# Optimization experiments

Measured on AMD Instinct MI355X. Metric: run time of the kernel, lower is better.

Reference implementation:

```python
import jax, jax.numpy as jnp
import numpy as np

F_DIM = 32          # phi_feature_dim
P = 128             # preselection_ap (spatial H=W)
NU = 4              # num_users
N1 = NU - 1         # n_cat1 == n_cat2
N3 = (NU - 1) ** 2  # n_cat3


def setup_inputs() -> dict:
    key = jax.random.key(0)
    k1, k2, k3, k4, k5 = jax.random.split(key, 5)
    B, CIN = 32, 8
    phi_input = jax.random.normal(k1, (B, CIN, P, P), dtype=jnp.float32)
    W1 = jax.random.normal(k2, (4 * F_DIM, CIN), dtype=jnp.float32) * 0.1
    b1 = jax.random.normal(k3, (4 * F_DIM,), dtype=jnp.float32) * 0.1
    W3 = jax.random.normal(k4, (4 * F_DIM, 4 * F_DIM), dtype=jnp.float32) * 0.1
    b3 = jax.random.normal(k5, (4 * F_DIM,), dtype=jnp.float32) * 0.1
    ex = jnp.ones((P, P), dtype=jnp.float32) - jnp.eye(P, dtype=jnp.float32)
    return {"phi_input": phi_input, "W1": W1, "b1": b1, "W3": W3, "b3": b3, "ex": ex}


def _conv1x1(x, W, b):
    # 1x1 conv == channel matmul: [b,c,h,w] x [o,c] -> [b,o,h,w]
    return jnp.einsum('bchw,oc->bohw', x, W) + b[None, :, None, None]


def _postprocess(r, ex):
    f = F_DIM
    c0 = r[:, :f]
    c1 = jnp.einsum('ph,bchw->bcpw', ex, r[:, f:2 * f]) / N1
    c2 = jnp.einsum('bchw,wq->bchq', r[:, 2 * f:3 * f], ex) / N1
    c3 = jnp.einsum('ph,bchw,wq->bcpq', ex, r[:, 3 * f:4 * f], ex) / N3
    return jnp.concatenate((c0, c1, c2, c3), axis=1)


def reference(phi_input, W1, b1, W3, b3, ex):
    r = jax.nn.relu(_conv1x1(phi_input, W1, b1))
    r = _postprocess(r, ex)
    r = jax.nn.relu(_conv1x1(r, W3, b3))
    r = _postprocess(r, ex)
    return r
```

## Files before the change

kernel.cpp:

```cpp
#include <hip/hip_runtime.h>
#include <stdint.h>

#define BATCH 32
#define CIN   8
#define NCH   128
#define PP    128
#define NSTRIP 8
#define KSTRIP 16

typedef __attribute__((ext_vector_type(8))) short    bf16x8;
typedef __attribute__((ext_vector_type(4))) float    f32x4;

__device__ __forceinline__ float bf2f(unsigned short u) {
    union { unsigned int i; float f; } x; x.i = ((unsigned int)u) << 16; return x.f;
}
__device__ __forceinline__ unsigned short f2bf(float f) {
    union { float f; unsigned int i; } x; x.f = f;
    unsigned int r = x.i + 0x7fffu + ((x.i >> 16) & 1u);
    return (unsigned short)(r >> 16);
}
__device__ __forceinline__ unsigned int pk2(float a, float b) {
    return (unsigned int)f2bf(a) | ((unsigned int)f2bf(b) << 16);
}

#define SWZB(row, cb) (((row) << 8) + ((cb) ^ (((row) & 7) << 4)))

__global__ __launch_bounds__(512, 4) void k1_sums(const float* __restrict__ phi,
        const float* __restrict__ W1, const float* __restrict__ b1,
        float* __restrict__ RS1t, float* __restrict__ CS1p) {
    __shared__ float cs_f[128 * 132];
    __shared__ unsigned short phi_b[2][1024];
    int bx = blockIdx.x;
    int b = bx >> 3, strip = bx & 7;
    int p0 = strip * 16;
    int tid = threadIdx.x;
    int wv = tid >> 6, l = tid & 63, lr = l & 15, lg = l >> 4;
    int c0 = wv * 16 + lg * 4;

    bf16x8 w1fr = {0, 0, 0, 0, 0, 0, 0, 0};
    if (lg == 0) {
        int cc = wv * 16 + lr;
        float4 wa = *(const float4*)(W1 + cc * 8);
        float4 wb = *(const float4*)(W1 + cc * 8 + 4);
        w1fr[0] = (short)f2bf(wa.x); w1fr[1] = (short)f2bf(wa.y);
        w1fr[2] = (short)f2bf(wa.z); w1fr[3] = (short)f2bf(wa.w);
        w1fr[4] = (short)f2bf(wb.x); w1fr[5] = (short)f2bf(wb.y);
        w1fr[6] = (short)f2bf(wb.z); w1fr[7] = (short)f2bf(wb.w);
    }
    f32x4 binit = {b1[c0], b1[c0 + 1], b1[c0 + 2], b1[c0 + 3]};
    if (tid < 128) {
        bf16x8 pv;
        #pragma unroll
        for (int ci = 0; ci < 8; ++ci)
            pv[ci] = (short)f2bf(phi[((size_t)(b * CIN + ci) * PP + p0) * PP + tid]);
        *(bf16x8*)(phi_b[0] + tid * 8) = pv;
    }
    __syncthreads();

    f32x4 cs_acc[8];
    #pragma unroll
    for (int i = 0; i < 8; ++i) { f32x4 z = {0.f, 0.f, 0.f, 0.f}; cs_acc[i] = z; }

    int cur = 0;
    for (int r = 0; r < 16; ++r) {
        int p = p0 + r;
        float pfv[8];
        if (r < 15 && tid < 128) {
            #pragma unroll
            for (int ci = 0; ci < 8; ++ci)
                pfv[ci] = phi[((size_t)(b * CIN + ci) * PP + p + 1) * PP + tid];
        }
        const unsigned short* pb = phi_b[cur];
        f32x4 rs4 = {0.f, 0.f, 0.f, 0.f};
        #pragma unroll
        for (int pt = 0; pt < 8; ++pt) {
            int pix = pt * 16 + lr;
            bf16x8 bfr1 = {0, 0, 0, 0, 0, 0, 0, 0};
            if (lg == 0) bfr1 = *(const bf16x8*)(pb + pix * 8);
            f32x4 a = __builtin_amdgcn_mfma_f32_16x16x32_bf16(w1fr, bfr1, binit, 0, 0, 0);
            f32x4 v = {fmaxf(a.x, 0.f), fmaxf(a.y, 0.f), fmaxf(a.z, 0.f), fmaxf(a.w, 0.f)};
            cs_acc[pt] += v;
            rs4 += v;
        }
        #pragma unroll
        for (int m = 1; m < 16; m <<= 1) {
            rs4.x += __shfl_xor(rs4.x, m);
            rs4.y += __shfl_xor(rs4.y, m);
            rs4.z += __shfl_xor(rs4.z, m);
            rs4.w += __shfl_xor(rs4.w, m);
        }
        if (lr == 0)
            *(f32x4*)(RS1t + ((size_t)b * PP + p) * NCH + c0) = rs4;
        if (r < 15 && tid < 128) {
            bf16x8 pv;
            #pragma unroll
            for (int ci = 0; ci < 8; ++ci) pv[ci] = (short)f2bf(pfv[ci]);
            *(bf16x8*)(phi_b[cur ^ 1] + tid * 8) = pv;
        }
        __syncthreads();
        cur ^= 1;
    }
    #pragma unroll
    for (int pt = 0; pt < 8; ++pt) {
        f32x4 v = cs_acc[pt];
        int q = pt * 16 + lr;
        cs_f[(c0 + 0) * 132 + q] = v.x;
        cs_f[(c0 + 1) * 132 + q] = v.y;
        cs_f[(c0 + 2) * 132 + q] = v.z;
        cs_f[(c0 + 3) * 132 + q] = v.w;
    }
    __syncthreads();
    float* dstp = CS1p + (size_t)(b * NSTRIP + strip) * NCH * PP;
    for (int k = tid; k < 16384; k += 512) {
        int cc = k >> 7, q = k & 127;
        dstp[k] = cs_f[cc * 132 + q];
    }
}

__global__ __launch_bounds__(256) void k1b_planes(const float* __restrict__ W3,
        const float* __restrict__ b3, const float* __restrict__ RS1t,
        const float* __restrict__ CS1p, float* __restrict__ Ap,
        float* __restrict__ Bqt, unsigned short* __restrict__ W3bf) {
    int bx = blockIdx.x;
    int b = bx >> 2, og = bx & 3;
    int tid = threadIdx.x;
    __shared__ float cs_g[64][132];
    __shared__ float rs_g[64][132];
    __shared__ float s1_96[32];
    for (int k = tid; k < 64 * 128; k += 256) {
        int r = k >> 7, q = k & 127;
        int ch_c = (r < 32) ? (32 + r) : (64 + r);
        float s = 0.f;
        #pragma unroll
        for (int s8 = 0; s8 < NSTRIP; ++s8)
            s += CS1p[((size_t)(b * NSTRIP + s8) * NCH + ch_c) * PP + q];
        cs_g[r][q] = s;
    }
    for (int k = tid; k < 64 * 128; k += 256) {
        int p = k >> 6, r = k & 63;
        rs_g[r][p] = RS1t[((size_t)b * PP + p) * NCH + 64 + r];
    }
    __syncthreads();
    if (tid < 32) {
        float s = 0.f;
        for (int q = 0; q < 128; ++q) s += cs_g[32 + tid][q];
        s1_96[tid] = s;
    }
    int o = og * 32 + (tid >> 3), qh = tid & 7;
    {
        float wa[64];
        #pragma unroll
        for (int r = 0; r < 64; ++r)
            wa[r] = (r < 32) ? W3[o * NCH + 32 + r] * (1.f / 3.f)
                             : -W3[o * NCH + 64 + r] * (1.f / 9.f);
        #pragma unroll
        for (int j = 0; j < 4; ++j) {
            int q = qh * 16 + j * 4;
            float4 a = {0.f, 0.f, 0.f, 0.f};
            #pragma unroll
            for (int r = 0; r < 64; ++r) {
                float4 cv = *(const float4*)&cs_g[r][q];
                a.x = fmaf(wa[r], cv.x, a.x);
                a.y = fmaf(wa[r], cv.y, a.y);
                a.z = fmaf(wa[r], cv.z, a.z);
                a.w = fmaf(wa[r], cv.w, a.w);
            }
            *(float4*)&Ap[((size_t)b * NCH + o) * PP + q] = a;
        }
    }
    __syncthreads();
    float cc = b3[o];
    #pragma unroll
    for (int r = 0; r < 32; ++r)
        cc = fmaf(W3[o * NCH + 96 + r] * (1.f / 9.f), s1_96[r], cc);
    {
        float wb[64];
        #pragma unroll
        for (int r = 0; r < 64; ++r)
            wb[r] = (r < 32) ? W3[o * NCH + 64 + r] * (1.f / 3.f)
                             : -W3[o * NCH + 64 + r] * (1.f / 9.f);
        #pragma unroll
        for (int j = 0; j < 4; ++j) {
            int p4 = qh * 16 + j * 4;
            float4 a = {0.f, 0.f, 0.f, 0.f};
            #pragma unroll
            for (int r = 0; r < 64; ++r) {
                float4 rv = *(const float4*)&rs_g[r][p4];
                a.x = fmaf(wb[r], rv.x, a.x);
                a.y = fmaf(wb[r], rv.y, a.y);
                a.z = fmaf(wb[r], rv.z, a.z);
                a.w = fmaf(wb[r], rv.w, a.w);
            }
            Bqt[((size_t)b * PP + p4 + 0) * NCH + o] = a.x + cc;
            Bqt[((size_t)b * PP + p4 + 1) * NCH + o] = a.y + cc;
            Bqt[((size_t)b * PP + p4 + 2) * NCH + o] = a.z + cc;
            Bqt[((size_t)b * PP + p4 + 3) * NCH + o] = a.w + cc;
        }
    }
    if (bx == 0) {
        for (int i = 0; i < 16; ++i) {
            int k = tid + i * 256;
            float4 w = *(const float4*)(W3 + k * 4);
            int c0 = (k * 4) & 127;
            float sc = (c0 < 32) ? 1.f : ((c0 < 96) ? (-1.f / 3.f) : (1.f / 9.f));
            unsigned int lo = pk2(w.x * sc, w.y * sc);
            unsigned int hi = pk2(w.z * sc, w.w * sc);
            uint2 u = {lo, hi};
            *(uint2*)(W3bf + k * 4) = u;
        }
    }
}

__global__ __launch_bounds__(512, 4) void k2_mfma(const float* __restrict__ phi,
        const float* __restrict__ W1, const float* __restrict__ b1,
        const unsigned short* __restrict__ W3bf,
        const float* __restrict__ Ap, const float* __restrict__ Bqt,
        unsigned short* __restrict__ v2) {
    int bx = blockIdx.x;
    int b = bx >> 4, strip = bx & 15;
    int p0 = strip * 8;
    __shared__ unsigned short w3_l[16384];
    __shared__ unsigned short t_l[16384];
    __shared__ unsigned short phi_b[2][1024];
    __shared__ float BC_l[2][128];
    int tid = threadIdx.x;
    int wv = tid >> 6, l = tid & 63, lr = l & 15, lg = l >> 4;
    int q0 = wv * 16 + lg * 4;

    #pragma unroll
    for (int i = 0; i < 4; ++i) {
        int k = tid + i * 512;
        int o = k >> 4, cb = (k & 15) * 16;
        bf16x8 v = *(const bf16x8*)(W3bf + k * 8);
        *(bf16x8*)((char*)w3_l + SWZB(o, cb)) = v;
    }
    bf16x8 w1fr = {0, 0, 0, 0, 0, 0, 0, 0};
    if (lg == 0) {
        int cc = wv * 16 + lr;
        float4 wa = *(const float4*)(W1 + cc * 8);
        float4 wb = *(const float4*)(W1 + cc * 8 + 4);
        w1fr[0] = (short)f2bf(wa.x); w1fr[1] = (short)f2bf(wa.y);
        w1fr[2] = (short)f2bf(wa.z); w1fr[3] = (short)f2bf(wa.w);
        w1fr[4] = (short)f2bf(wb.x); w1fr[5] = (short)f2bf(wb.y);
        w1fr[6] = (short)f2bf(wb.z); w1fr[7] = (short)f2bf(wb.w);
    }
    int c0 = wv * 16 + lg * 4;
    f32x4 binit = {b1[c0], b1[c0 + 1], b1[c0 + 2], b1[c0 + 3]};
    f32x4 apr[8];
    #pragma unroll
    for (int nt = 0; nt < 8; ++nt)
        apr[nt] = *(const f32x4*)(Ap + ((size_t)(b * NCH + nt * 16 + lr)) * PP + q0);
    if (tid < 128) {
        bf16x8 pv;
        #pragma unroll
        for (int ci = 0; ci < 8; ++ci)
            pv[ci] = (short)f2bf(phi[((size_t)(b * CIN + ci) * PP + p0) * PP + tid]);
        *(bf16x8*)(phi_b[0] + tid * 8) = pv;
        BC_l[0][tid] = Bqt[((size_t)b * PP + p0) * NCH + tid];
    }
    __syncthreads();

    for (int r = 0; r < 8; ++r) {
        int cur = r & 1, nxt = cur ^ 1;
        int p = p0 + r;
        float pfv[8]; float bcn = 0.f;
        if (r < 7 && tid < 128) {
            #pragma unroll
            for (int ci = 0; ci < 8; ++ci)
                pfv[ci] = phi[((size_t)(b * CIN + ci) * PP + p + 1) * PP + tid];
            bcn = Bqt[((size_t)b * PP + p + 1) * NCH + tid];
        }
        const unsigned short* pb = phi_b[cur];
        #pragma unroll
        for (int pt = 0; pt < 8; ++pt) {
            int pix = pt * 16 + lr;
            bf16x8 bfr1 = {0, 0, 0, 0, 0, 0, 0, 0};
            if (lg == 0) bfr1 = *(const bf16x8*)(pb + pix * 8);
            f32x4 a = __builtin_amdgcn_mfma_f32_16x16x32_bf16(w1fr, bfr1, binit, 0, 0, 0);
            uint2 u;
            u.x = pk2(fmaxf(a.x, 0.f), fmaxf(a.y, 0.f));
            u.y = pk2(fmaxf(a.z, 0.f), fmaxf(a.w, 0.f));
            *(uint2*)((char*)t_l + SWZB(pix, c0 * 2)) = u;
        }
        __syncthreads();
        bf16x8 afr[4];
        #pragma unroll
        for (int ks = 0; ks < 4; ++ks)
            afr[ks] = *(const bf16x8*)((char*)t_l + SWZB(wv * 16 + lr, ks * 64 + lg * 16));
        __syncthreads();
        #pragma unroll
        for (int nt = 0; nt < 8; ++nt) {
            int o = nt * 16 + lr;
            bf16x8 bfr[4];
            #pragma unroll
            for (int ks = 0; ks < 4; ++ks)
                bfr[ks] = *(const bf16x8*)((char*)w3_l + SWZB(o, ks * 64 + lg * 16));
            f32x4 acc = apr[nt] + BC_l[cur][o];
            #pragma unroll
            for (int ks = 0; ks < 4; ++ks)
                acc = __builtin_amdgcn_mfma_f32_16x16x32_bf16(afr[ks], bfr[ks], acc, 0, 0, 0);
            uint2 u;
            u.x = pk2(fmaxf(acc.x, 0.f), fmaxf(acc.y, 0.f));
            u.y = pk2(fmaxf(acc.z, 0.f), fmaxf(acc.w, 0.f));
            *(uint2*)((char*)t_l + SWZB(o, q0 * 2)) = u;
        }
        if (r < 7 && tid < 128) {
            bf16x8 pv;
            #pragma unroll
            for (int ci = 0; ci < 8; ++ci) pv[ci] = (short)f2bf(pfv[ci]);
            *(bf16x8*)(phi_b[nxt] + tid * 8) = pv;
            BC_l[nxt][tid] = bcn;
        }
        __syncthreads();
        #pragma unroll
        for (int i = 0; i < 4; ++i) {
            int k = tid + i * 512;
            int o = k >> 4, j = k & 15;
            bf16x8 v = *(const bf16x8*)((char*)t_l + SWZB(o, j * 16));
            *(bf16x8*)(v2 + ((size_t)(b * NCH + o) * PP + p) * PP + j * 8) = v;
        }
        __syncthreads();
    }
}

__global__ __launch_bounds__(256) void k3_out(const unsigned short* __restrict__ v2,
        float* __restrict__ out) {
    int bx = blockIdx.x;
    int b = bx >> 7, ch = bx & 127;
    int g = ch >> 5;
    __shared__ unsigned short v_l[128 * 136];
    __shared__ float rs_l[128], cs_l[128];
    __shared__ float s_sh;
    int tid = threadIdx.x;
    size_t base = (size_t)(b * NCH + ch) * (PP * PP);
    const unsigned short* src = v2 + base;
    #pragma unroll
    for (int i = 0; i < 8; ++i) {
        int k = tid + i * 256;
        int pr = k >> 4, c8 = k & 15;
        *(bf16x8*)(v_l + pr * 136 + c8 * 8) = *(const bf16x8*)(src + k * 8);
    }
    __syncthreads();
    if (tid < 128) {
        float s = 0.f;
        #pragma unroll 4
        for (int j = 0; j < 16; ++j) {
            bf16x8 u = *(const bf16x8*)(v_l + tid * 136 + j * 8);
            #pragma unroll
            for (int e = 0; e < 8; ++e) s += bf2f((unsigned short)u[e]);
        }
        rs_l[tid] = s;
    } else {
        int q = tid - 128;
        float s = 0.f;
        for (int pr = 0; pr < 128; ++pr) s += bf2f(v_l[pr * 136 + q]);
        cs_l[q] = s;
    }
    __syncthreads();
    if (tid < 64) {
        float s = rs_l[tid] + rs_l[tid + 64];
        #pragma unroll
        for (int off = 32; off > 0; off >>= 1) s += __shfl_down(s, off);
        if (tid == 0) s_sh = s;
    }
    __syncthreads();
    float stot = s_sh;
    float* dst = out + base;
    #pragma unroll
    for (int i = 0; i < 8; ++i) {
        int k = tid + i * 256;
        int pr = k >> 4, q0 = (k & 15) * 8;
        bf16x8 u = *(const bf16x8*)(v_l + pr * 136 + q0);
        float rp = rs_l[pr];
        float o8[8];
        #pragma unroll
        for (int e = 0; e < 8; ++e) {
            float v = bf2f((unsigned short)u[e]);
            float cq = cs_l[q0 + e];
            float r;
            if (g == 0)      r = v;
            else if (g == 1) r = (cq - v) * (1.f / 3.f);
            else if (g == 2) r = (rp - v) * (1.f / 3.f);
            else             r = ((stot - rp) - cq + v) * (1.f / 9.f);
            o8[e] = r;
        }
        f32x4 lo = {o8[0], o8[1], o8[2], o8[3]};
        f32x4 hi = {o8[4], o8[5], o8[6], o8[7]};
        *(f32x4*)(dst + pr * PP + q0)     = lo;
        *(f32x4*)(dst + pr * PP + q0 + 4) = hi;
    }
}

extern "C" void kernel_launch(void* const* d_in, const int* in_sizes, int n_in,
                              void* d_out, int out_size, void* d_ws, size_t ws_size,
                              hipStream_t stream) {
    (void)in_sizes; (void)n_in; (void)out_size; (void)ws_size;
    const float* phi = (const float*)d_in[0];
    const float* W1  = (const float*)d_in[1];
    const float* b1  = (const float*)d_in[2];
    const float* W3  = (const float*)d_in[3];
    const float* b3  = (const float*)d_in[4];
    float* out = (float*)d_out;

    char* ws = (char*)d_ws;
    size_t off = 0;
    unsigned short* v2 = (unsigned short*)(ws + off); off += (size_t)BATCH * NCH * PP * PP * 2;
    float* RS1t = (float*)(ws + off); off += (size_t)BATCH * NCH * PP * 4;
    float* CS1p = (float*)(ws + off); off += (size_t)BATCH * NSTRIP * NCH * PP * 4;
    float* Ap   = (float*)(ws + off); off += (size_t)BATCH * NCH * PP * 4;
    float* Bqt  = (float*)(ws + off); off += (size_t)BATCH * NCH * PP * 4;
    unsigned short* W3bf = (unsigned short*)(ws + off); off += (size_t)NCH * NCH * 2;

    k1_sums<<<BATCH * NSTRIP, 512, 0, stream>>>(phi, W1, b1, RS1t, CS1p);
    k1b_planes<<<BATCH * 4, 256, 0, stream>>>(W3, b3, RS1t, CS1p, Ap, Bqt, W3bf);
    k2_mfma<<<BATCH * KSTRIP, 512, 0, stream>>>(phi, W1, b1, W3bf, Ap, Bqt, v2);
    k3_out<<<BATCH * NCH, 256, 0, stream>>>(v2, out);
}
```

Measured before the change: 198.4 us.

## Hold W3 fragments in registers and double-buffer LDS; partial-sum reductions in k3

In k2, the W3 weight fragments are now loaded once into registers instead of being staged in shared memory and re-read every row. A separate LDS buffer holds the second-stage output, which lets two barriers per row be dropped. Launch bounds are relaxed to 2 blocks per CU to leave room for the larger register footprint. In k3, row and column sums are built from per-thread partial sums during the global load instead of copying the full tile into LDS, and the output pass re-reads v2 from global memory (likely served from cache). This trades occupancy and a second global read for fewer LDS accesses and fewer barriers.

After: 230.9 us. 1.16x slower.

```diff
diff --git a/kernel.cpp b/kernel.cpp
--- a/kernel.cpp
+++ b/kernel.cpp
@@ -211,7 +211,7 @@
     }
 }
 
-__global__ __launch_bounds__(512, 4) void k2_mfma(const float* __restrict__ phi,
+__global__ __launch_bounds__(512, 2) void k2_mfma(const float* __restrict__ phi,
         const float* __restrict__ W1, const float* __restrict__ b1,
         const unsigned short* __restrict__ W3bf,
         const float* __restrict__ Ap, const float* __restrict__ Bqt,
@@ -219,21 +219,21 @@
     int bx = blockIdx.x;
     int b = bx >> 4, strip = bx & 15;
     int p0 = strip * 8;
-    __shared__ unsigned short w3_l[16384];
     __shared__ unsigned short t_l[16384];
+    __shared__ unsigned short v_l[16384];
     __shared__ unsigned short phi_b[2][1024];
     __shared__ float BC_l[2][128];
     int tid = threadIdx.x;
     int wv = tid >> 6, l = tid & 63, lr = l & 15, lg = l >> 4;
     int q0 = wv * 16 + lg * 4;
-
-    #pragma unroll
-    for (int i = 0; i < 4; ++i) {
-        int k = tid + i * 512;
-        int o = k >> 4, cb = (k & 15) * 16;
-        bf16x8 v = *(const bf16x8*)(W3bf + k * 8);
-        *(bf16x8*)((char*)w3_l + SWZB(o, cb)) = v;
-    }
+    int c0 = q0;
+
+    bf16x8 w3r[8][4];
+    #pragma unroll
+    for (int nt = 0; nt < 8; ++nt)
+        #pragma unroll
+        for (int ks = 0; ks < 4; ++ks)
+            w3r[nt][ks] = *(const bf16x8*)(W3bf + (size_t)(nt * 16 + lr) * NCH + ks * 32 + lg * 8);
     bf16x8 w1fr = {0, 0, 0, 0, 0, 0, 0, 0};
     if (lg == 0) {
         int cc = wv * 16 + lr;
@@ -244,7 +244,6 @@
         w1fr[4] = (short)f2bf(wb.x); w1fr[5] = (short)f2bf(wb.y);
         w1fr[6] = (short)f2bf(wb.z); w1fr[7] = (short)f2bf(wb.w);
     }
-    int c0 = wv * 16 + lg * 4;
     f32x4 binit = {b1[c0], b1[c0 + 1], b1[c0 + 2], b1[c0 + 3]};
     f32x4 apr[8];
     #pragma unroll
@@ -287,22 +286,17 @@
         #pragma unroll
         for (int ks = 0; ks < 4; ++ks)
             afr[ks] = *(const bf16x8*)((char*)t_l + SWZB(wv * 16 + lr, ks * 64 + lg * 16));
-        __syncthreads();
         #pragma unroll
         for (int nt = 0; nt < 8; ++nt) {
             int o = nt * 16 + lr;
-            bf16x8 bfr[4];
+            f32x4 acc = apr[nt] + BC_l[cur][o];
             #pragma unroll
             for (int ks = 0; ks < 4; ++ks)
-                bfr[ks] = *(const bf16x8*)((char*)w3_l + SWZB(o, ks * 64 + lg * 16));
-            f32x4 acc = apr[nt] + BC_l[cur][o];
-            #pragma unroll
-            for (int ks = 0; ks < 4; ++ks)
-                acc = __builtin_amdgcn_mfma_f32_16x16x32_bf16(afr[ks], bfr[ks], acc, 0, 0, 0);
+                acc = __builtin_amdgcn_mfma_f32_16x16x32_bf16(afr[ks], w3r[nt][ks], acc, 0, 0, 0);
             uint2 u;
             u.x = pk2(fmaxf(acc.x, 0.f), fmaxf(acc.y, 0.f));
             u.y = pk2(fmaxf(acc.z, 0.f), fmaxf(acc.w, 0.f));
-            *(uint2*)((char*)t_l + SWZB(o, q0 * 2)) = u;
+            *(uint2*)((char*)v_l + SWZB(o, q0 * 2)) = u;
         }
         if (r < 7 && tid < 128) {
             bf16x8 pv;
@@ -316,10 +310,9 @@
         for (int i = 0; i < 4; ++i) {
             int k = tid + i * 512;
             int o = k >> 4, j = k & 15;
-            bf16x8 v = *(const bf16x8*)((char*)t_l + SWZB(o, j * 16));
+            bf16x8 v = *(const bf16x8*)((char*)v_l + SWZB(o, j * 16));
             *(bf16x8*)(v2 + ((size_t)(b * NCH + o) * PP + p) * PP + j * 8) = v;
         }
-        __syncthreads();
     }
 }
 
@@ -328,32 +321,46 @@
     int bx = blockIdx.x;
     int b = bx >> 7, ch = bx & 127;
     int g = ch >> 5;
-    __shared__ unsigned short v_l[128 * 136];
+    __shared__ float rsp[128][17];
+    __shared__ float csp[16][132];
     __shared__ float rs_l[128], cs_l[128];
     __shared__ float s_sh;
     int tid = threadIdx.x;
     size_t base = (size_t)(b * NCH + ch) * (PP * PP);
     const unsigned short* src = v2 + base;
+
+    int pc = tid >> 4, qc = tid & 15;
+    float cs8[8];
+    #pragma unroll
+    for (int e = 0; e < 8; ++e) cs8[e] = 0.f;
     #pragma unroll
     for (int i = 0; i < 8; ++i) {
-        int k = tid + i * 256;
-        int pr = k >> 4, c8 = k & 15;
-        *(bf16x8*)(v_l + pr * 136 + c8 * 8) = *(const bf16x8*)(src + k * 8);
-    }
+        int pr = pc * 8 + i;
+        bf16x8 u = *(const bf16x8*)(src + pr * PP + qc * 8);
+        float rp = 0.f;
+        #pragma unroll
+        for (int e = 0; e < 8; ++e) {
+            float v = bf2f((unsigned short)u[e]);
+            cs8[e] += v;
+            rp += v;
+        }
+        rsp[pr][qc] = rp;
+    }
+    f32x4 clo = {cs8[0], cs8[1], cs8[2], cs8[3]};
+    f32x4 chi = {cs8[4], cs8[5], cs8[6], cs8[7]};
+    *(f32x4*)&csp[pc][qc * 8]     = clo;
+    *(f32x4*)&csp[pc][qc * 8 + 4] = chi;
     __syncthreads();
     if (tid < 128) {
         float s = 0.f;
-        #pragma unroll 4
-        for (int j = 0; j < 16; ++j) {
-            bf16x8 u = *(const bf16x8*)(v_l + tid * 136 + j * 8);
-            #pragma unroll
-            for (int e = 0; e < 8; ++e) s += bf2f((unsigned short)u[e]);
-        }
+        #pragma unroll
+        for (int j = 0; j < 16; ++j) s += rsp[tid][j];
         rs_l[tid] = s;
     } else {
         int q = tid - 128;
         float s = 0.f;
-        for (int pr = 0; pr < 128; ++pr) s += bf2f(v_l[pr * 136 + q]);
+        #pragma unroll
+        for (int i = 0; i < 16; ++i) s += csp[i][q];
         cs_l[q] = s;
     }
     __syncthreads();
@@ -370,7 +377,7 @@
     for (int i = 0; i < 8; ++i) {
         int k = tid + i * 256;
         int pr = k >> 4, q0 = (k & 15) * 8;
-        bf16x8 u = *(const bf16x8*)(v_l + pr * 136 + q0);
+        bf16x8 u = *(const bf16x8*)(src + pr * PP + q0);
         float rp = rs_l[pr];
         float o8[8];
         #pragma unroll
```

## Compute row/column sums of second-stage activations in k2 instead of k3

Applied to the files above, without the earlier changes.

The producer kernel now accumulates per-row sums and per-strip column sums of channel groups 1-3 while it writes the bf16 intermediate. A small new kernel reduces the strip partials, and k3 reads the precomputed sums. This removes k3's LDS staging and its serial 128-step column reductions, so k3 becomes a simple streaming elementwise pass. In exchange it adds an extra launch, partial-sum traffic, and more register pressure in k2, where the occupancy hint in launch bounds was also dropped.

Measured after the change: 221.5 us. 11.7% more time.

```diff
diff --git a/kernel.cpp b/kernel.cpp
--- a/kernel.cpp
+++ b/kernel.cpp
@@ -211,11 +211,12 @@
     }
 }
 
-__global__ __launch_bounds__(512, 4) void k2_mfma(const float* __restrict__ phi,
+__global__ __launch_bounds__(512) void k2_mfma(const float* __restrict__ phi,
         const float* __restrict__ W1, const float* __restrict__ b1,
         const unsigned short* __restrict__ W3bf,
         const float* __restrict__ Ap, const float* __restrict__ Bqt,
-        unsigned short* __restrict__ v2) {
+        unsigned short* __restrict__ v2, float* __restrict__ RSvT,
+        float* __restrict__ CSp) {
     int bx = blockIdx.x;
     int b = bx >> 4, strip = bx & 15;
     int p0 = strip * 8;
@@ -226,6 +227,7 @@
     int tid = threadIdx.x;
     int wv = tid >> 6, l = tid & 63, lr = l & 15, lg = l >> 4;
     int q0 = wv * 16 + lg * 4;
+    int g16 = tid >> 4, jj = tid & 15;
 
     #pragma unroll
     for (int i = 0; i < 4; ++i) {
@@ -260,6 +262,10 @@
     }
     __syncthreads();
 
+    float cs1[8], cs3[8];
+    #pragma unroll
+    for (int e = 0; e < 8; ++e) { cs1[e] = 0.f; cs3[e] = 0.f; }
+
     for (int r = 0; r < 8; ++r) {
         int cur = r & 1, nxt = cur ^ 1;
         int p = p0 + r;
@@ -312,66 +318,101 @@
             BC_l[nxt][tid] = bcn;
         }
         __syncthreads();
+        float rsum2 = 0.f, rsum3 = 0.f;
         #pragma unroll
         for (int i = 0; i < 4; ++i) {
             int k = tid + i * 512;
             int o = k >> 4, j = k & 15;
             bf16x8 v = *(const bf16x8*)((char*)t_l + SWZB(o, j * 16));
             *(bf16x8*)(v2 + ((size_t)(b * NCH + o) * PP + p) * PP + j * 8) = v;
-        }
-        __syncthreads();
+            if (i == 1) {
+                #pragma unroll
+                for (int e = 0; e < 8; ++e) cs1[e] += bf2f((unsigned short)v[e]);
+            } else if (i == 2) {
+                #pragma unroll
+                for (int e = 0; e < 8; ++e) rsum2 += bf2f((unsigned short)v[e]);
+            } else if (i == 3) {
+                #pragma unroll
+                for (int e = 0; e < 8; ++e) {
+                    float f = bf2f((unsigned short)v[e]);
+                    cs3[e] += f; rsum3 += f;
+                }
+            }
+        }
+        #pragma unroll
+        for (int m = 1; m < 16; m <<= 1) {
+            rsum2 += __shfl_xor(rsum2, m);
+            rsum3 += __shfl_xor(rsum3, m);
+        }
+        if (jj == 0) {
+            RSvT[((size_t)b * 64 + g16) * PP + p]      = rsum2;
+            RSvT[((size_t)b * 64 + 32 + g16) * PP + p] = rsum3;
+        }
+        __syncthreads();
+    }
+    {
+        float* dst = CSp + ((size_t)(b * KSTRIP + strip)) * 64 * PP;
+        f32x4 a = {cs1[0], cs1[1], cs1[2], cs1[3]};
+        f32x4 c = {cs1[4], cs1[5], cs1[6], cs1[7]};
+        *(f32x4*)(dst + (size_t)g16 * PP + jj * 8)     = a;
+        *(f32x4*)(dst + (size_t)g16 * PP + jj * 8 + 4) = c;
+        f32x4 d = {cs3[0], cs3[1], cs3[2], cs3[3]};
+        f32x4 e = {cs3[4], cs3[5], cs3[6], cs3[7]};
+        *(f32x4*)(dst + (size_t)(32 + g16) * PP + jj * 8)     = d;
+        *(f32x4*)(dst + (size_t)(32 + g16) * PP + jj * 8 + 4) = e;
+    }
+}
+
+__global__ __launch_bounds__(256) void k2s_reduce(const float* __restrict__ CSp,
+        float* __restrict__ CSv) {
+    int bx = blockIdx.x;
+    int b = bx >> 3, grp = bx & 7;
+    int tid = threadIdx.x;
+    #pragma unroll
+    for (int it = 0; it < 4; ++it) {
+        int jc = grp * 8 + it * 2 + (tid >> 7);
+        int q = tid & 127;
+        float s = 0.f;
+        #pragma unroll
+        for (int st = 0; st < KSTRIP; ++st)
+            s += CSp[(((size_t)(b * KSTRIP + st)) * 64 + jc) * PP + q];
+        CSv[((size_t)b * 64 + jc) * PP + q] = s;
     }
 }
 
 __global__ __launch_bounds__(256) void k3_out(const unsigned short* __restrict__ v2,
+        const float* __restrict__ RSvT, const float* __restrict__ CSv,
         float* __restrict__ out) {
     int bx = blockIdx.x;
     int b = bx >> 7, ch = bx & 127;
     int g = ch >> 5;
-    __shared__ unsigned short v_l[128 * 136];
     __shared__ float rs_l[128], cs_l[128];
-    __shared__ float s_sh;
+    __shared__ float part[4];
     int tid = threadIdx.x;
     size_t base = (size_t)(b * NCH + ch) * (PP * PP);
     const unsigned short* src = v2 + base;
-    #pragma unroll
-    for (int i = 0; i < 8; ++i) {
-        int k = tid + i * 256;
-        int pr = k >> 4, c8 = k & 15;
-        *(bf16x8*)(v_l + pr * 136 + c8 * 8) = *(const bf16x8*)(src + k * 8);
-    }
-    __syncthreads();
+    float* dst = out + base;
     if (tid < 128) {
-        float s = 0.f;
-        #pragma unroll 4
-        for (int j = 0; j < 16; ++j) {
-            bf16x8 u = *(const bf16x8*)(v_l + tid * 136 + j * 8);
-            #pragma unroll
-            for (int e = 0; e < 8; ++e) s += bf2f((unsigned short)u[e]);
-        }
-        rs_l[tid] = s;
-    } else {
-        int q = tid - 128;
-        float s = 0.f;
-        for (int pr = 0; pr < 128; ++pr) s += bf2f(v_l[pr * 136 + q]);
-        cs_l[q] = s;
-    }
-    __syncthreads();
-    if (tid < 64) {
-        float s = rs_l[tid] + rs_l[tid + 64];
-        #pragma unroll
-        for (int off = 32; off > 0; off >>= 1) s += __shfl_down(s, off);
-        if (tid == 0) s_sh = s;
-    }
-    __syncthreads();
-    float stot = s_sh;
-    float* dst = out + base;
+        if (g >= 2) rs_l[tid] = RSvT[((size_t)b * 64 + (ch - 64)) * PP + tid];
+        if (g == 1) cs_l[tid] = CSv[((size_t)b * 64 + (ch - 32)) * PP + tid];
+        if (g == 3) cs_l[tid] = CSv[((size_t)b * 64 + 32 + (ch - 96)) * PP + tid];
+    }
+    __syncthreads();
+    float stot = 0.f;
+    if (g == 3) {
+        float s = (tid < 128) ? cs_l[tid] : 0.f;
+        #pragma unroll
+        for (int m = 1; m < 64; m <<= 1) s += __shfl_xor(s, m);
+        if ((tid & 63) == 0) part[tid >> 6] = s;
+        __syncthreads();
+        stot = part[0] + part[1];
+    }
     #pragma unroll
     for (int i = 0; i < 8; ++i) {
         int k = tid + i * 256;
         int pr = k >> 4, q0 = (k & 15) * 8;
-        bf16x8 u = *(const bf16x8*)(v_l + pr * 136 + q0);
-        float rp = rs_l[pr];
+        bf16x8 u = *(const bf16x8*)(src + pr * PP + q0);
+        float rp = (g >= 2) ? rs_l[pr] : 0.f;
         float o8[8];
         #pragma unroll
         for (int e = 0; e < 8; ++e) {
@@ -410,9 +451,13 @@
     float* Ap   = (float*)(ws + off); off += (size_t)BATCH * NCH * PP * 4;
     float* Bqt  = (float*)(ws + off); off += (size_t)BATCH * NCH * PP * 4;
     unsigned short* W3bf = (unsigned short*)(ws + off); off += (size_t)NCH * NCH * 2;
+    float* RSvT = (float*)(ws + off); off += (size_t)BATCH * 64 * PP * 4;
+    float* CSp  = (float*)(ws + off); off += (size_t)BATCH * KSTRIP * 64 * PP * 4;
+    float* CSv  = (float*)(ws + off); off += (size_t)BATCH * 64 * PP * 4;
 
     k1_sums<<<BATCH * NSTRIP, 512, 0, stream>>>(phi, W1, b1, RS1t, CS1p);
     k1b_planes<<<BATCH * 4, 256, 0, stream>>>(W3, b3, RS1t, CS1p, Ap, Bqt, W3bf);
-    k2_mfma<<<BATCH * KSTRIP, 512, 0, stream>>>(phi, W1, b1, W3bf, Ap, Bqt, v2);
-    k3_out<<<BATCH * NCH, 256, 0, stream>>>(v2, out);
-}
+    k2_mfma<<<BATCH * KSTRIP, 512, 0, stream>>>(phi, W1, b1, W3bf, Ap, Bqt, v2, RSvT, CSp);
+    k2s_reduce<<<BATCH * 8, 256, 0, stream>>>(CSp, CSv);
+    k3_out<<<BATCH * NCH, 256, 0, stream>>>(v2, RSvT, CSv, out);
+}
```
